# Kernel tuning notes

Hardware: AMD Instinct MI355X
Metric: run time of the kernel (lower is better)

The kernel has to match this reference:

```python
import jax, jax.numpy as jnp
import numpy as np

N, L, E, H = 4, 2048, 1024, 16
DK = E // H  # 64

def setup_inputs() -> dict:
    key = jax.random.key(0)
    ks = jax.random.split(key, 5)
    scale = 0.02
    return {
        "x": jax.random.normal(ks[0], (N, L, E), dtype=jnp.float32),
        "Wq": jax.random.normal(ks[1], (E, E), dtype=jnp.float32) * scale,
        "Wk": jax.random.normal(ks[2], (E, E), dtype=jnp.float32) * scale,
        "Wv": jax.random.normal(ks[3], (E, E), dtype=jnp.float32) * scale,
        "Wo": jax.random.normal(ks[4], (E, E), dtype=jnp.float32) * scale,
    }

def reference(x, Wq, Wk, Wv, Wo):
    n, l, _ = x.shape
    # nn.Linear(bias=False): y = x @ W.T
    q = x @ Wq.T  # (n, l, H*DK)
    k = x @ Wk.T
    v = x @ Wv.T
    # Faithful to torch .view: plain reshape (NOT transpose-based head split)
    q = q.reshape(n, H, l, DK)
    k = k.reshape(n, H, l, DK)
    v = v.reshape(n, H, l, DK)
    scores = jnp.einsum('nhqd,nhkd->nhqk', q, k) / jnp.sqrt(jnp.float32(DK))
    attn = jax.nn.softmax(scores, axis=-1)
    out = jnp.einsum('nhqk,nhkd->nhqd', attn, v).reshape(n, l, H * DK)
    return out @ Wo.T
```

## Files before the change

### kernel.cpp

```cpp
#include <hip/hip_runtime.h>


#define DEVI __device__ __forceinline__

typedef _Float16 half8 __attribute__((ext_vector_type(8)));
typedef _Float16 half4v __attribute__((ext_vector_type(4)));
typedef float f32x4 __attribute__((ext_vector_type(4)));

DEVI void gload_lds16(const void* g, void* l) {
    __builtin_amdgcn_global_load_lds(
        (const __attribute__((address_space(1))) void*)g,
        (__attribute__((address_space(3))) void*)l,
        16, 0, 0);
}

DEVI f32x4 zero4() { f32x4 z = {0.f, 0.f, 0.f, 0.f}; return z; }

#if __has_builtin(__builtin_amdgcn_exp2f)
DEVI float fast_exp2(float x) { return __builtin_amdgcn_exp2f(x); }
#else
DEVI float fast_exp2(float x) { return exp2f(x); }
#endif

DEVI half8 lds_read8_swz(const _Float16* base, int row, int colbyte) {
    const char* p = (const char*)base;
    const int off = (row * 128 + colbyte) ^ ((row & 7) << 4);
    return *(const half8*)(p + off);
}

__global__ __launch_bounds__(256) void f2h_kernel(const float* __restrict__ s,
                                                  _Float16* __restrict__ d) {
    const size_t i = (size_t)blockIdx.x * 256 + threadIdx.x;
    const float4 v = ((const float4*)s)[i];
    half4v h;
    h[0] = (_Float16)v.x; h[1] = (_Float16)v.y;
    h[2] = (_Float16)v.z; h[3] = (_Float16)v.w;
    ((half4v*)d)[i] = h;
}

template<int OUT_F32>
__global__ __launch_bounds__(256) void gemm_nt(const _Float16* __restrict__ A,
                                               const _Float16* __restrict__ B,
                                               void* __restrict__ Cout,
                                               int M, int N, int K, float alpha) {
    alignas(16) __shared__ _Float16 As[128 * 64];
    alignas(16) __shared__ _Float16 Bs[128 * 64];
    const int t = threadIdx.x;
    const int lane = t & 63;
    const int w = t >> 6;
    const int wr = (w >> 1) * 64;
    const int wc = (w & 1) * 64;
    const int bm = blockIdx.y * 128;
    const int bn = blockIdx.x * 128;
    const int r16 = lane & 15;
    const int q4 = lane >> 4;
    const int sr = t >> 3;
    const int sc8 = (t & 7) * 8;

    f32x4 acc[4][4];
    #pragma unroll
    for (int mi = 0; mi < 4; ++mi)
        #pragma unroll
        for (int ni = 0; ni < 4; ++ni)
            acc[mi][ni] = zero4();

    for (int kt = 0; kt < K; kt += 64) {
        #pragma unroll
        for (int i = 0; i < 4; ++i) {
            gload_lds16(A + (size_t)(bm + i * 32 + sr) * K + kt + sc8, &As[i * 2048 + t * 8]);
            gload_lds16(B + (size_t)(bn + i * 32 + sr) * K + kt + sc8, &Bs[i * 2048 + t * 8]);
        }
        __syncthreads();
        #pragma unroll
        for (int kk = 0; kk < 2; ++kk) {
            half8 a[4], b[4];
            #pragma unroll
            for (int mi = 0; mi < 4; ++mi)
                a[mi] = *(const half8*)&As[(wr + mi * 16 + r16) * 64 + kk * 32 + q4 * 8];
            #pragma unroll
            for (int ni = 0; ni < 4; ++ni)
                b[ni] = *(const half8*)&Bs[(wc + ni * 16 + r16) * 64 + kk * 32 + q4 * 8];
            #pragma unroll
            for (int mi = 0; mi < 4; ++mi)
                #pragma unroll
                for (int ni = 0; ni < 4; ++ni)
                    acc[mi][ni] = __builtin_amdgcn_mfma_f32_16x16x32_f16(a[mi], b[ni], acc[mi][ni], 0, 0, 0);
        }
        __syncthreads();
    }
    #pragma unroll
    for (int mi = 0; mi < 4; ++mi) {
        const int row = bm + wr + mi * 16 + q4 * 4;
        #pragma unroll
        for (int ni = 0; ni < 4; ++ni) {
            const int col = bn + wc + ni * 16 + r16;
            #pragma unroll
            for (int i = 0; i < 4; ++i) {
                const float v = acc[mi][ni][i] * alpha;
                if (OUT_F32)
                    ((float*)Cout)[(size_t)(row + i) * N + col] = v;
                else
                    ((_Float16*)Cout)[(size_t)(row + i) * N + col] = (_Float16)v;
            }
        }
    }
}

__global__ __launch_bounds__(256) void transpose_v(const _Float16* __restrict__ V,
                                                   _Float16* __restrict__ Vt) {
    __shared__ unsigned short lds[64 * 65];
    const int t = threadIdx.x;
    const int kt = blockIdx.x;
    const size_t hb = (size_t)blockIdx.y * 131072;
    const int r = t >> 2;
    const int c0 = (t & 3) * 16;
    const unsigned short* Vi = (const unsigned short*)V;
    #pragma unroll
    for (int j = 0; j < 2; ++j) {
        union { uint4 u; unsigned short s[8]; } tmp;
        tmp.u = *(const uint4*)&Vi[hb + (size_t)(kt * 64 + r) * 64 + c0 + j * 8];
        #pragma unroll
        for (int e = 0; e < 8; ++e)
            lds[r * 65 + c0 + j * 8 + e] = tmp.s[e];
    }
    __syncthreads();
    unsigned short* Vo = (unsigned short*)Vt;
    #pragma unroll
    for (int j = 0; j < 16; ++j) {
        const int idx = j * 256 + t;
        const int d = idx >> 6;
        const int c = idx & 63;
        Vo[hb + (size_t)d * 2048 + kt * 64 + c] = lds[c * 65 + d];
    }
}

__global__ __launch_bounds__(256) void attn_kernel(const _Float16* __restrict__ Q,
                                                   const _Float16* __restrict__ K,
                                                   const _Float16* __restrict__ Vt,
                                                   _Float16* __restrict__ O) {
    alignas(16) __shared__ _Float16 Ks[2][64 * 64];
    alignas(16) __shared__ _Float16 Vs[2][64 * 64];
    alignas(16) __shared__ _Float16 Ps[4][32 * 64];
    const int t = threadIdx.x;
    const int lane = t & 63;
    const int w = t >> 6;
    const size_t hb = (size_t)blockIdx.y * 131072;
    const int qt = blockIdx.x;
    const int r16 = lane & 15;
    const int q4 = lane >> 4;
    const int sr = t >> 3;
    const int sc = t & 7;

    half8 aq[2][2];
    const int q0 = qt * 128 + w * 32;
    #pragma unroll
    for (int mi = 0; mi < 2; ++mi)
        #pragma unroll
        for (int kk = 0; kk < 2; ++kk)
            aq[mi][kk] = *(const half8*)&Q[hb + (size_t)(q0 + mi * 16 + r16) * 64 + kk * 32 + q4 * 8];

    f32x4 o[2][4];
    float lsum[2][4];
    #pragma unroll
    for (int mi = 0; mi < 2; ++mi)
        #pragma unroll
        for (int i = 0; i < 4; ++i) lsum[mi][i] = 0.f;
    #pragma unroll
    for (int mi = 0; mi < 2; ++mi)
        #pragma unroll
        for (int ni = 0; ni < 4; ++ni)
            o[mi][ni] = zero4();

    _Float16* Pw = Ps[w];

    const int R0 = sr, R1 = 32 + sr;
    const int scs0 = (sc ^ (R0 & 7)) * 8;
    const int scs1 = (sc ^ (R1 & 7)) * 8;

    {
        gload_lds16(&K[hb + (size_t)R0 * 64 + scs0],        &Ks[0][t * 8]);
        gload_lds16(&K[hb + (size_t)R1 * 64 + scs1],        &Ks[0][2048 + t * 8]);
        gload_lds16(&Vt[hb + (size_t)R0 * 2048 + scs0],     &Vs[0][t * 8]);
        gload_lds16(&Vt[hb + (size_t)R1 * 2048 + scs1],     &Vs[0][2048 + t * 8]);
    }
    __syncthreads();

    int pb = 0;
    for (int kt = 0; kt < 32; ++kt) {
        if (kt + 1 < 32) {
            const size_t kb = hb + (size_t)(kt + 1) * 64 * 64;
            gload_lds16(&K[kb + (size_t)R0 * 64 + scs0],                 &Ks[pb ^ 1][t * 8]);
            gload_lds16(&K[kb + (size_t)R1 * 64 + scs1],                 &Ks[pb ^ 1][2048 + t * 8]);
            gload_lds16(&Vt[hb + (size_t)R0 * 2048 + (kt + 1) * 64 + scs0], &Vs[pb ^ 1][t * 8]);
            gload_lds16(&Vt[hb + (size_t)R1 * 2048 + (kt + 1) * 64 + scs1], &Vs[pb ^ 1][2048 + t * 8]);
        }

        f32x4 s[2][4];
        #pragma unroll
        for (int mi = 0; mi < 2; ++mi)
            #pragma unroll
            for (int ni = 0; ni < 4; ++ni)
                s[mi][ni] = zero4();
        __builtin_amdgcn_s_setprio(1);
        #pragma unroll
        for (int kk = 0; kk < 2; ++kk) {
            half8 bk[4];
            #pragma unroll
            for (int ni = 0; ni < 4; ++ni)
                bk[ni] = lds_read8_swz(Ks[pb], ni * 16 + r16, (kk * 32 + q4 * 8) * 2);
            #pragma unroll
            for (int mi = 0; mi < 2; ++mi)
                #pragma unroll
                for (int ni = 0; ni < 4; ++ni)
                    s[mi][ni] = __builtin_amdgcn_mfma_f32_16x16x32_f16(aq[mi][kk], bk[ni], s[mi][ni], 0, 0, 0);
        }
        __builtin_amdgcn_s_setprio(0);

        #pragma unroll
        for (int mi = 0; mi < 2; ++mi)
            #pragma unroll
            for (int i = 0; i < 4; ++i) {
                const int pr = mi * 16 + q4 * 4 + i;
                float rs = 0.f;
                #pragma unroll
                for (int ni = 0; ni < 4; ++ni) {
                    const float p = fast_exp2(s[mi][ni][i]);
                    rs += p;
                    const int off = ((pr * 128 + (ni * 16 + r16) * 2) ^ ((pr & 7) << 4));
                    *(_Float16*)((char*)Pw + off) = (_Float16)p;
                }
                lsum[mi][i] += rs;
            }

        __builtin_amdgcn_s_setprio(1);
        #pragma unroll
        for (int kk = 0; kk < 2; ++kk) {
            half8 ap[2], bv[4];
            #pragma unroll
            for (int mi = 0; mi < 2; ++mi)
                ap[mi] = lds_read8_swz(Pw, mi * 16 + r16, (kk * 32 + q4 * 8) * 2);
            #pragma unroll
            for (int ni = 0; ni < 4; ++ni)
                bv[ni] = lds_read8_swz(Vs[pb], ni * 16 + r16, (kk * 32 + q4 * 8) * 2);
            #pragma unroll
            for (int mi = 0; mi < 2; ++mi)
                #pragma unroll
                for (int ni = 0; ni < 4; ++ni)
                    o[mi][ni] = __builtin_amdgcn_mfma_f32_16x16x32_f16(ap[mi], bv[ni], o[mi][ni], 0, 0, 0);
        }
        __builtin_amdgcn_s_setprio(0);

        __syncthreads();
        pb ^= 1;
    }

    #pragma unroll
    for (int mi = 0; mi < 2; ++mi)
        #pragma unroll
        for (int i = 0; i < 4; ++i) {
            float l = lsum[mi][i];
            l += __shfl_xor(l, 1);
            l += __shfl_xor(l, 2);
            l += __shfl_xor(l, 4);
            l += __shfl_xor(l, 8);
            const float inv = 1.f / l;
            const int row = q0 + mi * 16 + q4 * 4 + i;
            #pragma unroll
            for (int ni = 0; ni < 4; ++ni)
                O[hb + (size_t)row * 64 + ni * 16 + r16] = (_Float16)(o[mi][ni][i] * inv);
        }
}

extern "C" void kernel_launch(void* const* d_in, const int* in_sizes, int n_in,
                              void* d_out, int out_size, void* d_ws, size_t ws_size,
                              hipStream_t stream) {
    const float* x  = (const float*)d_in[0];
    const float* Wq = (const float*)d_in[1];
    const float* Wk = (const float*)d_in[2];
    const float* Wv = (const float*)d_in[3];
    const float* Wo = (const float*)d_in[4];
    float* out = (float*)d_out;

    const size_t XSZ = (size_t)8192 * 1024;
    const size_t WSZ = (size_t)1024 * 1024;

    _Float16* ws  = (_Float16*)d_ws;
    _Float16* xh  = ws;
    _Float16* wqh = ws + XSZ;
    _Float16* wkh = wqh + WSZ;
    _Float16* wvh = wkh + WSZ;
    _Float16* woh = wvh + WSZ;
    _Float16* qh  = woh + WSZ;
    _Float16* kh  = qh + XSZ;
    _Float16* vh  = kh + XSZ;
    _Float16* aoh = vh + XSZ;
    _Float16* vth = xh;

    f2h_kernel<<<XSZ / 4 / 256, 256, 0, stream>>>(x,  xh);
    f2h_kernel<<<WSZ / 4 / 256, 256, 0, stream>>>(Wq, wqh);
    f2h_kernel<<<WSZ / 4 / 256, 256, 0, stream>>>(Wk, wkh);
    f2h_kernel<<<WSZ / 4 / 256, 256, 0, stream>>>(Wv, wvh);
    f2h_kernel<<<WSZ / 4 / 256, 256, 0, stream>>>(Wo, woh);

    const float qscale = 0.125f * 1.44269504088896340736f;
    dim3 gg(1024 / 128, 8192 / 128);
    gemm_nt<0><<<gg, 256, 0, stream>>>(xh, wqh, (void*)qh, 8192, 1024, 1024, qscale);
    gemm_nt<0><<<gg, 256, 0, stream>>>(xh, wkh, (void*)kh, 8192, 1024, 1024, 1.0f);
    gemm_nt<0><<<gg, 256, 0, stream>>>(xh, wvh, (void*)vh, 8192, 1024, 1024, 1.0f);

    transpose_v<<<dim3(32, 64), 256, 0, stream>>>(vh, vth);

    attn_kernel<<<dim3(16, 64), 256, 0, stream>>>(qh, kh, vth, aoh);

    gemm_nt<1><<<gg, 256, 0, stream>>>(aoh, woh, d_out, 8192, 1024, 1024, 1.0f);
    (void)out; (void)in_sizes; (void)n_in; (void)out_size; (void)ws_size;
}
```

Before: 339.2 us.

## Fuse QKV projections into one GEMM launch and remap blocks XCD-aware

Replaces the three separate Q/K/V projection GEMMs with a single launch that treats the contiguous Wq/Wk/Wv fp16 buffers as one 3072-row weight matrix, routing each output tile to the q/k/v buffer and applying the Q scale per tile. All GEMM and attention grids become 1D with a block-index remapping meant to keep neighbouring tiles on the same XCD, improving L2 reuse of shared A rows and K/V heads. It also removes two launches and their tail effects, but hardcodes all problem dimensions.

Measured after the change: 309.5 us. -8.7%, faster.

```diff
diff --git a/kernel.cpp b/kernel.cpp
--- a/kernel.cpp
+++ b/kernel.cpp
@@ -38,11 +38,13 @@
     ((half4v*)d)[i] = h;
 }
 
-template<int OUT_F32>
-__global__ __launch_bounds__(256) void gemm_nt(const _Float16* __restrict__ A,
-                                               const _Float16* __restrict__ B,
-                                               void* __restrict__ Cout,
-                                               int M, int N, int K, float alpha) {
+template<int MODE>
+__global__ __launch_bounds__(256) void gemm_k(const _Float16* __restrict__ A,
+                                              const _Float16* __restrict__ B,
+                                              void* __restrict__ Cout,
+                                              float qscale) {
+    constexpr int NBLK = (MODE == 0) ? 24 : 8;
+    constexpr int CPX  = (MODE == 0) ? 192 : 64;
     alignas(16) __shared__ _Float16 As[128 * 64];
     alignas(16) __shared__ _Float16 Bs[128 * 64];
     const int t = threadIdx.x;
@@ -50,8 +52,9 @@
     const int w = t >> 6;
     const int wr = (w >> 1) * 64;
     const int wc = (w & 1) * 64;
-    const int bm = blockIdx.y * 128;
-    const int bn = blockIdx.x * 128;
+    const int nid = (blockIdx.x & 7) * CPX + (blockIdx.x >> 3);
+    const int bn = (nid % NBLK) * 128;
+    const int bm = (nid / NBLK) * 128;
     const int r16 = lane & 15;
     const int q4 = lane >> 4;
     const int sr = t >> 3;
@@ -64,11 +67,11 @@
         for (int ni = 0; ni < 4; ++ni)
             acc[mi][ni] = zero4();
 
-    for (int kt = 0; kt < K; kt += 64) {
+    for (int kt = 0; kt < 1024; kt += 64) {
         #pragma unroll
         for (int i = 0; i < 4; ++i) {
-            gload_lds16(A + (size_t)(bm + i * 32 + sr) * K + kt + sc8, &As[i * 2048 + t * 8]);
-            gload_lds16(B + (size_t)(bn + i * 32 + sr) * K + kt + sc8, &Bs[i * 2048 + t * 8]);
+            gload_lds16(A + (size_t)(bm + i * 32 + sr) * 1024 + kt + sc8, &As[i * 2048 + t * 8]);
+            gload_lds16(B + (size_t)(bn + i * 32 + sr) * 1024 + kt + sc8, &Bs[i * 2048 + t * 8]);
         }
         __syncthreads();
         #pragma unroll
@@ -88,19 +91,33 @@
         }
         __syncthreads();
     }
-    #pragma unroll
-    for (int mi = 0; mi < 4; ++mi) {
-        const int row = bm + wr + mi * 16 + q4 * 4;
-        #pragma unroll
-        for (int ni = 0; ni < 4; ++ni) {
-            const int col = bn + wc + ni * 16 + r16;
-            #pragma unroll
-            for (int i = 0; i < 4; ++i) {
-                const float v = acc[mi][ni][i] * alpha;
-                if (OUT_F32)
-                    ((float*)Cout)[(size_t)(row + i) * N + col] = v;
-                else
-                    ((_Float16*)Cout)[(size_t)(row + i) * N + col] = (_Float16)v;
+    if (MODE == 0) {
+        const int which = bn >> 10;
+        const int cb = bn & 1023;
+        const float alpha = (which == 0) ? qscale : 1.0f;
+        _Float16* C = (_Float16*)Cout + (size_t)which * 8388608;
+        #pragma unroll
+        for (int mi = 0; mi < 4; ++mi) {
+            const int row = bm + wr + mi * 16 + q4 * 4;
+            #pragma unroll
+            for (int ni = 0; ni < 4; ++ni) {
+                const int col = cb + wc + ni * 16 + r16;
+                #pragma unroll
+                for (int i = 0; i < 4; ++i)
+                    C[(size_t)(row + i) * 1024 + col] = (_Float16)(acc[mi][ni][i] * alpha);
+            }
+        }
+    } else {
+        float* C = (float*)Cout;
+        #pragma unroll
+        for (int mi = 0; mi < 4; ++mi) {
+            const int row = bm + wr + mi * 16 + q4 * 4;
+            #pragma unroll
+            for (int ni = 0; ni < 4; ++ni) {
+                const int col = bn + wc + ni * 16 + r16;
+                #pragma unroll
+                for (int i = 0; i < 4; ++i)
+                    C[(size_t)(row + i) * 1024 + col] = acc[mi][ni][i];
             }
         }
     }
@@ -144,8 +161,9 @@
     const int t = threadIdx.x;
     const int lane = t & 63;
     const int w = t >> 6;
-    const size_t hb = (size_t)blockIdx.y * 131072;
-    const int qt = blockIdx.x;
+    const int nid = (blockIdx.x & 7) * 128 + (blockIdx.x >> 3);
+    const size_t hb = (size_t)(nid >> 4) * 131072;
+    const int qt = nid & 15;
     const int r16 = lane & 15;
     const int q4 = lane >> 4;
     const int sr = t >> 3;
@@ -279,7 +297,6 @@
     const float* Wk = (const float*)d_in[2];
     const float* Wv = (const float*)d_in[3];
     const float* Wo = (const float*)d_in[4];
-    float* out = (float*)d_out;
 
     const size_t XSZ = (size_t)8192 * 1024;
     const size_t WSZ = (size_t)1024 * 1024;
@@ -303,15 +320,13 @@
     f2h_kernel<<<WSZ / 4 / 256, 256, 0, stream>>>(Wo, woh);
 
     const float qscale = 0.125f * 1.44269504088896340736f;
-    dim3 gg(1024 / 128, 8192 / 128);
-    gemm_nt<0><<<gg, 256, 0, stream>>>(xh, wqh, (void*)qh, 8192, 1024, 1024, qscale);
-    gemm_nt<0><<<gg, 256, 0, stream>>>(xh, wkh, (void*)kh, 8192, 1024, 1024, 1.0f);
-    gemm_nt<0><<<gg, 256, 0, stream>>>(xh, wvh, (void*)vh, 8192, 1024, 1024, 1.0f);
+
+    gemm_k<0><<<1536, 256, 0, stream>>>(xh, wqh, (void*)qh, qscale);
 
     transpose_v<<<dim3(32, 64), 256, 0, stream>>>(vh, vth);
 
-    attn_kernel<<<dim3(16, 64), 256, 0, stream>>>(qh, kh, vth, aoh);
-
-    gemm_nt<1><<<gg, 256, 0, stream>>>(aoh, woh, d_out, 8192, 1024, 1024, 1.0f);
-    (void)out; (void)in_sizes; (void)n_in; (void)out_size; (void)ws_size;
-}
+    attn_kernel<<<1024, 256, 0, stream>>>(qh, kh, vth, aoh);
+
+    gemm_k<1><<<512, 256, 0, stream>>>(aoh, woh, d_out, 1.0f);
+    (void)in_sizes; (void)n_in; (void)out_size; (void)ws_size;
+}
```
